# Performance work log

Measured on AMD Instinct MI355X. Metric: run time of the kernel, lower is better.

The kernel has to match this reference:

```python
import jax, jax.numpy as jnp
import numpy as np

SIDE_LEN = 128
RESOLUTION = 1.0  # Angstrom per pixel


def setup_inputs() -> dict:
    key = jax.random.key(0)
    k1, k2, k3 = jax.random.split(key, 3)
    B, A = 16, 20000
    # atom xyz coords in Angstrom, spread within the field of view (+/- 63.5 A)
    mol = jax.random.normal(k1, (B, A, 3), dtype=jnp.float32) * 20.0
    # per-atom Gaussian std in [0.5, 1.5) A (strictly positive)
    stds = jax.random.uniform(k2, (A,), dtype=jnp.float32) + 0.5
    # per-atom density (mass) in [0.5, 1.5)
    densities = jax.random.uniform(k3, (A,), dtype=jnp.float32) + 0.5
    return {"mol": mol, "stds": stds, "densities": densities}


def reference(mol, stds, densities):
    # Pixel-center coordinate grid, identical to torch.arange(-x_max, x_max+1e-5, res)
    x_max = (SIDE_LEN - 1) * RESOLUTION / 2
    coord = jnp.arange(-x_max, x_max + 1e-5, RESOLUTION, dtype=jnp.float32)  # (S,)
    var = stds * stds                              # (A,)
    neg_half_inv_var = (-0.5 / var)[None, :, None] # (1,A,1)
    # Separable Gaussian profiles: exp(-(coord - mu)^2 / (2 var))
    dx = coord[None, None, :] - mol[:, :, 0:1]     # (B,A,S) x-offsets
    dy = coord[None, None, :] - mol[:, :, 1:2]     # (B,A,S) y-offsets
    gx = jnp.exp(neg_half_inv_var * dx * dx)       # (B,A,W)
    gy = jnp.exp(neg_half_inv_var * dy * dy)       # (B,A,H)
    coef = densities / (2.0 * jnp.pi * var)        # (A,)
    # img[b,h,w] = sum_a coef_a * gy[b,a,h] * gx[b,a,w]  (batched matmul)
    img = jnp.einsum('bah,baw->bhw', gy * coef[None, :, None], gx)
    return img  # (B, SIDE_LEN, SIDE_LEN)
```

## Files before the change

### kernel.cpp

```cpp
#include <hip/hip_runtime.h>


#define S 128
#define NS 32
#define PER 640
#define QS 2
#define BLOCK 256

typedef _Float16 f16;
typedef _Float16 f16x2 __attribute__((ext_vector_type(2)));
typedef _Float16 f16x8 __attribute__((ext_vector_type(8)));
typedef float floatx16 __attribute__((ext_vector_type(16)));

#if __has_builtin(__builtin_amdgcn_exp2f)
#define FAST_EXP2(x) __builtin_amdgcn_exp2f(x)
#else
#define FAST_EXP2(x) exp2f(x)
#endif
#if __has_builtin(__builtin_amdgcn_rcpf)
#define FAST_RCP(x) __builtin_amdgcn_rcpf(x)
#else
#define FAST_RCP(x) (1.0f / (x))
#endif

static __device__ __forceinline__ f16x2 PKRTZ(float a, float b) {
#if __has_builtin(__builtin_amdgcn_cvt_pkrtz)
    return __builtin_bit_cast(f16x2, __builtin_amdgcn_cvt_pkrtz(a, b));
#else
    return (f16x2){(f16)a, (f16)b};
#endif
}

union frag_u { f16x8 v; f16x2 h[4]; };

__global__ __launch_bounds__(BLOCK, 4) void k_proj(
    const float* __restrict__ mol,
    const float* __restrict__ stds,
    const float* __restrict__ dens,
    f16* __restrict__ part,
    int B, int A)
{
    __shared__ float4 sP[PER];

    const int ks   = blockIdx.x;
    const int q    = blockIdx.y;
    const int b    = blockIdx.z;
    const int tid  = threadIdx.x;
    const int lane = tid & 63;
    const int wav  = tid >> 6;
    const int l31  = lane & 31;
    const int hi   = lane >> 5;

    const int a0  = ks * PER;
    const int a1  = min(a0 + PER, A);
    const int cnt = a1 - a0;

    for (int i = tid; i < cnt; i += BLOCK) {
        const int a = a0 + i;
        const size_t idx = (size_t)b * A + a;
        float x  = mol[idx * 3 + 0];
        float y  = mol[idx * 3 + 1];
        float v  = stds[a] * stds[a];
        float rv = FAST_RCP(v);
        sP[i] = make_float4(x, y, -0.72134752044448f * rv,
                            __log2f(dens[a] * 0.15915494309189535f * rv));
    }
    __syncthreads();

    const float py0 = (float)(q * 64 + l31) - 63.5f;
    const float px0 = (float)(wav * 32 + l31) - 63.5f;

    floatx16 acc0 = {0.f}, acc1 = {0.f};

    const int nk = cnt >> 4;
    const float4* sp = sP + hi * 8;

    for (int s = 0; s < nk; ++s) {
        const float4* pp = sp + (size_t)s * 16;
        frag_u A0, A1, B0;
#pragma unroll
        for (int jp = 0; jp < 4; ++jp) {
            float ea0[2], ea1[2], eb0[2];
#pragma unroll
            for (int u = 0; u < 2; ++u) {
                float4 p = pp[2 * jp + u];
                float dy = py0 - p.y;
                float t  = p.z * dy;
                float g0 = fmaf(t, dy, p.w);
                float g1 = fmaf(1024.0f, p.z, fmaf(64.0f, t, g0));
                ea0[u] = FAST_EXP2(g0);
                ea1[u] = FAST_EXP2(g1);
                float dx = px0 - p.x;
                eb0[u] = FAST_EXP2((p.z * dx) * dx);
            }
            A0.h[jp] = PKRTZ(ea0[0], ea0[1]);
            A1.h[jp] = PKRTZ(ea1[0], ea1[1]);
            B0.h[jp] = PKRTZ(eb0[0], eb0[1]);
        }
        acc0 = __builtin_amdgcn_mfma_f32_32x32x16_f16(A0.v, B0.v, acc0, 0, 0, 0);
        acc1 = __builtin_amdgcn_mfma_f32_32x32x16_f16(A1.v, B0.v, acc1, 0, 0, 0);
    }

    f16* base = part + ((size_t)(b * NS + ks)) * (S * S) + lane * 16;
    floatx16 accs[2] = {acc0, acc1};
#pragma unroll
    for (int rr = 0; rr < 2; ++rr) {
        f16* pq = base + (size_t)((q * 2 + rr) * 4 + wav) * 1024;
        frag_u lo, hiv;
#pragma unroll
        for (int jp = 0; jp < 4; ++jp) {
            lo.h[jp]  = PKRTZ(accs[rr][2 * jp],     accs[rr][2 * jp + 1]);
            hiv.h[jp] = PKRTZ(accs[rr][2 * jp + 8], accs[rr][2 * jp + 9]);
        }
        *(f16x8*)(pq + 0) = lo.v;
        *(f16x8*)(pq + 8) = hiv.v;
    }
}

__global__ __launch_bounds__(256) void k_reduce(const f16* __restrict__ part,
                                                float* __restrict__ out) {
    const int b  = blockIdx.z;
    const int f8 = (blockIdx.x * 256 + threadIdx.x) * 8;

    const f16* src = part + (size_t)b * NS * (S * S) + f8;
    float s0[8] = {0.f}, s1[8] = {0.f};
    for (int s = 0; s < NS; s += 2) {
        f16x8 v0 = *(const f16x8*)&src[(size_t)s * (S * S)];
        f16x8 v1 = *(const f16x8*)&src[(size_t)(s + 1) * (S * S)];
#pragma unroll
        for (int i = 0; i < 8; ++i) { s0[i] += (float)v0[i]; s1[i] += (float)v1[i]; }
    }

    const int reg0 = f8 & 15;
    const int lane = (f8 >> 4) & 63;
    const int tile = f8 >> 10;
    const int r    = tile >> 2;
    const int cc   = tile & 3;
    const int rowb = r * 32 + 4 * (lane >> 5);
    const int col  = cc * 32 + (lane & 31);
#pragma unroll
    for (int i = 0; i < 8; ++i) {
        const int reg = reg0 + i;
        const int row = rowb + (reg & 3) + 8 * (reg >> 2);
        out[((size_t)b * S + row) * S + col] = s0[i] + s1[i];
    }
}

extern "C" void kernel_launch(void* const* d_in, const int* in_sizes, int n_in,
                              void* d_out, int out_size, void* d_ws, size_t ws_size,
                              hipStream_t stream) {
    const float* mol  = (const float*)d_in[0];
    const float* stds = (const float*)d_in[1];
    const float* dens = (const float*)d_in[2];
    float* out = (float*)d_out;

    const int A = in_sizes[1];
    const int B = in_sizes[0] / (A * 3);

    f16* part = (f16*)d_ws;

    k_proj<<<dim3(NS, QS, B), dim3(BLOCK), 0, stream>>>(mol, stds, dens, part, B, A);
    k_reduce<<<dim3((S * S) / (256 * 8), 1, B), dim3(256), 0, stream>>>(part, out);
}
```

Measured before the change: 103.8 us.

## Give each wave a 64x64 output tile and split atoms across wave halves

Each wave now computes a 64x64 tile using four MFMA accumulators, reusing both the A and B exp fragments. This cuts the exp work per output compared with the earlier 64x32 tiles, where the y-profiles were recomputed in two separate blocks. The block grows to 512 threads: two halves of waves each process half of the atom chunk, and their partials are summed through 64KB of shared memory before the f16 store. This removes the q grid dimension. The cost is more accumulator registers, lower occupancy from the large LDS buffer, and an extra LDS reduction with a barrier.

```diff
diff --git a/kernel.cpp b/kernel.cpp
--- a/kernel.cpp
+++ b/kernel.cpp
@@ -4,8 +4,7 @@
 #define S 128
 #define NS 32
 #define PER 640
-#define QS 2
-#define BLOCK 256
+#define BLOCK 512
 
 typedef _Float16 f16;
 typedef _Float16 f16x2 __attribute__((ext_vector_type(2)));
@@ -41,13 +40,15 @@
     int B, int A)
 {
     __shared__ float4 sP[PER];
+    __shared__ float red[4 * 4096];
 
     const int ks   = blockIdx.x;
-    const int q    = blockIdx.y;
-    const int b    = blockIdx.z;
+    const int b    = blockIdx.y;
     const int tid  = threadIdx.x;
     const int lane = tid & 63;
     const int wav  = tid >> 6;
+    const int quad = wav & 3;
+    const int half = wav >> 2;
     const int l31  = lane & 31;
     const int hi   = lane >> 5;
 
@@ -67,20 +68,26 @@
     }
     __syncthreads();
 
-    const float py0 = (float)(q * 64 + l31) - 63.5f;
-    const float px0 = (float)(wav * 32 + l31) - 63.5f;
+    const int hcnt = cnt >> 1;
+    const int nk   = hcnt >> 4;
 
-    floatx16 acc0 = {0.f}, acc1 = {0.f};
+    const float py0 = (float)((quad >> 1) * 64 + l31) - 63.5f;
+    const float px0 = (float)((quad & 1) * 64 + l31) - 63.5f;
 
-    const int nk = cnt >> 4;
-    const float4* sp = sP + hi * 8;
+    floatx16 acc[2][2];
+#pragma unroll
+    for (int rr = 0; rr < 2; ++rr)
+#pragma unroll
+        for (int cb = 0; cb < 2; ++cb) acc[rr][cb] = (floatx16){0.f};
+
+    const float4* sp = sP + half * hcnt + hi * 8;
 
     for (int s = 0; s < nk; ++s) {
         const float4* pp = sp + (size_t)s * 16;
-        frag_u A0, A1, B0;
+        frag_u A0, A1, B0, B1;
 #pragma unroll
         for (int jp = 0; jp < 4; ++jp) {
-            float ea0[2], ea1[2], eb0[2];
+            float ea0[2], ea1[2], eb0[2], eb1[2];
 #pragma unroll
             for (int u = 0; u < 2; ++u) {
                 float4 p = pp[2 * jp + u];
@@ -91,29 +98,57 @@
                 ea0[u] = FAST_EXP2(g0);
                 ea1[u] = FAST_EXP2(g1);
                 float dx = px0 - p.x;
-                eb0[u] = FAST_EXP2((p.z * dx) * dx);
+                float sx = p.z * dx;
+                float h0 = sx * dx;
+                float h1 = fmaf(1024.0f, p.z, fmaf(64.0f, sx, h0));
+                eb0[u] = FAST_EXP2(h0);
+                eb1[u] = FAST_EXP2(h1);
             }
             A0.h[jp] = PKRTZ(ea0[0], ea0[1]);
             A1.h[jp] = PKRTZ(ea1[0], ea1[1]);
             B0.h[jp] = PKRTZ(eb0[0], eb0[1]);
+            B1.h[jp] = PKRTZ(eb1[0], eb1[1]);
         }
-        acc0 = __builtin_amdgcn_mfma_f32_32x32x16_f16(A0.v, B0.v, acc0, 0, 0, 0);
-        acc1 = __builtin_amdgcn_mfma_f32_32x32x16_f16(A1.v, B0.v, acc1, 0, 0, 0);
+        acc[0][0] = __builtin_amdgcn_mfma_f32_32x32x16_f16(A0.v, B0.v, acc[0][0], 0, 0, 0);
+        acc[0][1] = __builtin_amdgcn_mfma_f32_32x32x16_f16(A0.v, B1.v, acc[0][1], 0, 0, 0);
+        acc[1][0] = __builtin_amdgcn_mfma_f32_32x32x16_f16(A1.v, B0.v, acc[1][0], 0, 0, 0);
+        acc[1][1] = __builtin_amdgcn_mfma_f32_32x32x16_f16(A1.v, B1.v, acc[1][1], 0, 0, 0);
     }
 
-    f16* base = part + ((size_t)(b * NS + ks)) * (S * S) + lane * 16;
-    floatx16 accs[2] = {acc0, acc1};
+    float* rq = red + quad * 4096;
+    if (half == 0) {
 #pragma unroll
-    for (int rr = 0; rr < 2; ++rr) {
-        f16* pq = base + (size_t)((q * 2 + rr) * 4 + wav) * 1024;
-        frag_u lo, hiv;
+        for (int rr = 0; rr < 2; ++rr)
 #pragma unroll
-        for (int jp = 0; jp < 4; ++jp) {
-            lo.h[jp]  = PKRTZ(accs[rr][2 * jp],     accs[rr][2 * jp + 1]);
-            hiv.h[jp] = PKRTZ(accs[rr][2 * jp + 8], accs[rr][2 * jp + 9]);
-        }
-        *(f16x8*)(pq + 0) = lo.v;
-        *(f16x8*)(pq + 8) = hiv.v;
+            for (int cb = 0; cb < 2; ++cb) {
+                float* t = rq + (rr * 2 + cb) * 1024 + lane;
+#pragma unroll
+                for (int j = 0; j < 16; ++j) t[j * 64] = acc[rr][cb][j];
+            }
+    }
+    __syncthreads();
+
+    if (half == 1) {
+        f16* base = part + ((size_t)(b * NS + ks)) * (S * S) + lane * 16;
+#pragma unroll
+        for (int rr = 0; rr < 2; ++rr)
+#pragma unroll
+            for (int cb = 0; cb < 2; ++cb) {
+                float* t = rq + (rr * 2 + cb) * 1024 + lane;
+                floatx16 v = acc[rr][cb];
+#pragma unroll
+                for (int j = 0; j < 16; ++j) v[j] += t[j * 64];
+                const int tileidx = ((quad >> 1) * 2 + rr) * 4 + ((quad & 1) * 2 + cb);
+                f16* pq = base + (size_t)tileidx * 1024;
+                frag_u lo, hiv;
+#pragma unroll
+                for (int jp = 0; jp < 4; ++jp) {
+                    lo.h[jp]  = PKRTZ(v[2 * jp],     v[2 * jp + 1]);
+                    hiv.h[jp] = PKRTZ(v[2 * jp + 8], v[2 * jp + 9]);
+                }
+                *(f16x8*)(pq + 0) = lo.v;
+                *(f16x8*)(pq + 8) = hiv.v;
+            }
     }
 }
 
@@ -159,6 +194,6 @@
 
     f16* part = (f16*)d_ws;
 
-    k_proj<<<dim3(NS, QS, B), dim3(BLOCK), 0, stream>>>(mol, stds, dens, part, B, A);
+    k_proj<<<dim3(NS, B), dim3(BLOCK), 0, stream>>>(mol, stds, dens, part, B, A);
     k_reduce<<<dim3((S * S) / (256 * 8), 1, B), dim3(256), 0, stream>>>(part, out);
 }
```

Measured after the change: 93.54 us (median of 2 runs). 9.9% less time.
